# Kernel optimization log

Measured on AMD Instinct MI355X. Metric: run time of the kernel, lower is better.

## Reference

```python
import jax, jax.numpy as jnp
import numpy as np

H_DIM = 1024
HEAD_SIZE = 1024


def setup_inputs() -> dict:
    key = jax.random.key(0)
    ks = jax.random.split(key, 7)
    s = 1.0 / np.sqrt(H_DIM)
    x = jax.random.normal(ks[0], (4, 4096, H_DIM), dtype=jnp.float32)
    Wq = jax.random.uniform(ks[1], (H_DIM, HEAD_SIZE), jnp.float32, -s, s)
    bq = jax.random.uniform(ks[2], (HEAD_SIZE,), jnp.float32, -s, s)
    Wk = jax.random.uniform(ks[3], (H_DIM, HEAD_SIZE), jnp.float32, -s, s)
    bk = jax.random.uniform(ks[4], (HEAD_SIZE,), jnp.float32, -s, s)
    Wv = jax.random.uniform(ks[5], (H_DIM, HEAD_SIZE), jnp.float32, -s, s)
    bv = jax.random.uniform(ks[6], (HEAD_SIZE,), jnp.float32, -s, s)
    return {"x": x, "Wq": Wq, "bq": bq, "Wk": Wk, "bk": bk, "Wv": Wv, "bv": bv}


def reference(x, Wq, bq, Wk, bk, Wv, bv):
    B, S, _ = x.shape
    q = x @ Wq + bq  # [B,S,hs]
    k = x @ Wk + bk
    v = x @ Wv + bv
    scores = jnp.einsum('bqd,bkd->bqk', q, k)  # [B,S,S]
    causal = jnp.tril(jnp.ones((S, S), dtype=bool))
    scores = jnp.where(causal, scores, -jnp.inf)
    # original divides after masking; -inf stays -inf so math is identical
    w = jax.nn.softmax(scores / jnp.sqrt(jnp.float32(HEAD_SIZE)), axis=-1)
    # dropout p=0.0 -> identity
    return jnp.einsum('bqk,bkd->bqd', w, v)
```

## Files before the change

kernel.cpp:

```cpp
#include <hip/hip_runtime.h>
#include <stdint.h>

typedef _Float16 f16;
typedef _Float16 v8h __attribute__((ext_vector_type(8)));
typedef _Float16 v4h __attribute__((ext_vector_type(4)));
typedef float v4f __attribute__((ext_vector_type(4)));

#define LOG2E 1.44269504088896340736f
#define PT 16384

__device__ __forceinline__ void gll16(const void* g, void* l) {
  __builtin_amdgcn_global_load_lds((__attribute__((address_space(1))) void*)g,
                                   (__attribute__((address_space(3))) void*)l,
                                   16, 0, 0);
}

__device__ __forceinline__ int xcd_swz(int p, int chunk) {
  return (p & 7) * chunk + (p >> 3);
}

__global__ void k_cvt_x(const float* __restrict__ x, f16* __restrict__ xh, int n4) {
  int i = blockIdx.x * blockDim.x + threadIdx.x;
  if (i >= n4) return;
  float4 v = ((const float4*)x)[i];
  v4h o;
  o[0] = (f16)v.x; o[1] = (f16)v.y; o[2] = (f16)v.z; o[3] = (f16)v.w;
  ((v4h*)xh)[i] = o;
}

__global__ void k_cvt_wt(const float* __restrict__ Wq, const float* __restrict__ Wk,
                         const float* __restrict__ Wv, f16* __restrict__ Wt) {
  __shared__ f16 tile[64][65];
  int z = blockIdx.z;
  const float* W = (z == 0) ? Wq : (z == 1) ? Wk : Wv;
  int k0 = blockIdx.y * 64, n0 = blockIdx.x * 64;
  int t = threadIdx.x;
  int r = t >> 4, c4 = t & 15;
  for (int i = 0; i < 4; ++i) {
    int row = r + i * 16;
    float4 v = *(const float4*)&W[(size_t)(k0 + row) * 1024 + n0 + c4 * 4];
    tile[c4 * 4 + 0][row] = (f16)v.x;
    tile[c4 * 4 + 1][row] = (f16)v.y;
    tile[c4 * 4 + 2][row] = (f16)v.z;
    tile[c4 * 4 + 3][row] = (f16)v.w;
  }
  __syncthreads();
  f16* out = Wt + (size_t)z * 1048576;
  for (int i = 0; i < 4; ++i) {
    int n = r + i * 16;
    v4h o;
    o[0] = tile[n][c4 * 4 + 0];
    o[1] = tile[n][c4 * 4 + 1];
    o[2] = tile[n][c4 * 4 + 2];
    o[3] = tile[n][c4 * 4 + 3];
    *(v4h*)&out[(size_t)(n0 + n) * 1024 + k0 + c4 * 4] = o;
  }
}

__global__ __launch_bounds__(512) void k_qkv(
    const f16* __restrict__ xh,
    const f16* __restrict__ Wt,
    const float* __restrict__ bq, const float* __restrict__ bk, const float* __restrict__ bv,
    f16* __restrict__ q, f16* __restrict__ k, f16* __restrict__ vT) {
  __shared__ __align__(16) f16 As[2][16384];
  __shared__ __align__(16) f16 Bs[2][16384];
  int p = blockIdx.x + 64 * (blockIdx.y + 4 * blockIdx.z);
  int l = xcd_swz(p, 96);
  int mt = l / 12;
  int rem = l - mt * 12;
  int z = rem >> 2, nt = rem & 3;
  int m0 = mt * 256, n0 = nt * 256;
  const f16* gA = xh + (size_t)m0 * 1024;
  const f16* gB = Wt + (size_t)z * 1048576 + (size_t)n0 * 1024;
  const float* bias = (z == 0) ? bq : (z == 1) ? bk : bv;
  int tid = threadIdx.x;
  int lane = tid & 63, wave = tid >> 6;
  int quad = lane >> 4, l15 = lane & 15;
  int wm = (wave >> 2) * 128, wn = (wave & 3) * 64;

  int soff[4], slds[4];
#pragma unroll
  for (int h = 0; h < 4; ++h) {
    int s = h * 512 + tid;
    int row = s >> 3;
    int c = (s & 7) ^ (row & 7);
    soff[h] = row * 1024 + c * 8;
    slds[h] = (h * 512 + wave * 64) * 8;
  }
  v4f acc[8][4] = {};

#define QKV_STAGE(bb, kt_) do { int kk_ = (kt_) * 64;                      \
    _Pragma("unroll") for (int h = 0; h < 4; ++h)                          \
      gll16(gA + soff[h] + kk_, &As[bb][slds[h]]);                         \
    _Pragma("unroll") for (int h = 0; h < 4; ++h)                          \
      gll16(gB + soff[h] + kk_, &Bs[bb][slds[h]]);                         \
  } while (0)

#define QKV_COMPUTE(bb) do {                                               \
    _Pragma("unroll") for (int ks = 0; ks < 2; ++ks) {                     \
      int sl = ((ks * 4 + quad) ^ (l15 & 7)) * 8;                          \
      v8h a[8], bfr[4];                                                    \
      _Pragma("unroll") for (int i = 0; i < 8; ++i)                        \
        a[i] = *(const v8h*)&As[bb][(wm + i * 16 + l15) * 64 + sl];        \
      _Pragma("unroll") for (int j = 0; j < 4; ++j)                        \
        bfr[j] = *(const v8h*)&Bs[bb][(wn + j * 16 + l15) * 64 + sl];      \
      __builtin_amdgcn_s_setprio(1);                                       \
      _Pragma("unroll") for (int i = 0; i < 8; ++i)                        \
        _Pragma("unroll") for (int j = 0; j < 4; ++j)                      \
          acc[i][j] = __builtin_amdgcn_mfma_f32_16x16x32_f16(a[i], bfr[j], acc[i][j], 0, 0, 0); \
      __builtin_amdgcn_s_setprio(0);                                       \
      __builtin_amdgcn_s_barrier();                                        \
    }                                                                      \
  } while (0)

  QKV_STAGE(0, 0);
  QKV_STAGE(1, 1);
  int cur = 0;
#pragma unroll 1
  for (int kt = 0; kt < 15; ++kt) {
    asm volatile("s_waitcnt vmcnt(8)" ::: "memory");
    __builtin_amdgcn_s_barrier();
    QKV_COMPUTE(cur);
    if (kt + 2 < 16) QKV_STAGE(cur, kt + 2);
    cur ^= 1;
  }
  asm volatile("s_waitcnt vmcnt(0)" ::: "memory");
  __builtin_amdgcn_s_barrier();
  QKV_COMPUTE(cur);

  if (z < 2) {
    f16* outp = (z == 0) ? q : k;
    float scale = (z == 0) ? 0.03125f : 1.0f;
#pragma unroll
    for (int j = 0; j < 4; ++j) {
      int n = n0 + wn + j * 16 + l15;
      float bia = bias[n];
#pragma unroll
      for (int i = 0; i < 8; ++i) {
        int mb = m0 + wm + i * 16 + quad * 4;
#pragma unroll
        for (int r = 0; r < 4; ++r)
          outp[(size_t)(mb + r) * 1024 + n] = (f16)((acc[i][j][r] + bia) * scale);
      }
    }
  } else {
#pragma unroll
    for (int j = 0; j < 4; ++j) {
      int n = n0 + wn + j * 16 + l15;
      float bia = bias[n];
#pragma unroll
      for (int i = 0; i < 8; ++i) {
        int m = m0 + wm + i * 16 + quad * 4;
        int bb = m >> 12, s = m & 4095;
        v4h o;
#pragma unroll
        for (int r = 0; r < 4; ++r) o[r] = (f16)(acc[i][j][r] + bia);
        *(v4h*)&vT[((size_t)bb * 1024 + n) * 4096 + s] = o;
      }
    }
  }
#undef QKV_STAGE
#undef QKV_COMPUTE
}

__global__ void k_zero(float* __restrict__ p) {
  p[blockIdx.x * 256 + threadIdx.x] = 0.f;
}

__global__ __launch_bounds__(256) void k_sgemm(
    const f16* __restrict__ q, const f16* __restrict__ kmat,
    f16* __restrict__ P, float* __restrict__ rowsum, int b0) {
  __shared__ __align__(16) f16 As[128 * 32];
  __shared__ __align__(16) f16 Bs[128 * 32];
  int p = blockIdx.x + 528 * blockIdx.y;
  int l = xcd_swz(p, 132);
  int i = (l >= 528) ? l - 528 : l;
  int bb = (l >= 528) ? 1 : 0;
  int b = b0 * 2 + bb;
  int mt = (int)((sqrtf(8.f * i + 1.f) - 1.f) * 0.5f);
  while ((mt + 1) * (mt + 2) / 2 <= i) ++mt;
  while (mt * (mt + 1) / 2 > i) --mt;
  int nt = i - mt * (mt + 1) / 2;
  const f16* A = q + ((size_t)b * 4096 + (size_t)mt * 128) * 1024;
  const f16* B = kmat + ((size_t)b * 4096 + (size_t)nt * 128) * 1024;
  f16* Pt = P + (size_t)bb * 528 * PT + (size_t)i * PT;

  int tid = threadIdx.x;
  int lane = tid & 63, wave = tid >> 6;
  int quad = lane >> 4, l15 = lane & 15;
  int wm = (wave & 1) * 64, wn = (wave >> 1) * 64;
  v4f acc[4][4] = {};

  for (int kk = 0; kk < 1024; kk += 32) {
    __syncthreads();
    for (int h = 0; h < 2; ++h) {
      int s = h * 256 + tid;
      int row = s >> 2, pos = s & 3;
      int c = pos ^ (row & 3);
      gll16(&A[(size_t)row * 1024 + kk + c * 8], &As[(h * 256 + wave * 64) * 8]);
    }
    for (int h = 0; h < 2; ++h) {
      int s = h * 256 + tid;
      int row = s >> 2, pos = s & 3;
      int c = pos ^ (row & 3);
      gll16(&B[(size_t)row * 1024 + kk + c * 8], &Bs[(h * 256 + wave * 64) * 8]);
    }
    __syncthreads();
    v8h a[4], bf[4];
    for (int ii = 0; ii < 4; ++ii) {
      int rowa = wm + ii * 16 + l15;
      int pa = quad ^ (rowa & 3);
      a[ii] = *(const v8h*)&As[rowa * 32 + pa * 8];
      int rowb = wn + ii * 16 + l15;
      int pb = quad ^ (rowb & 3);
      bf[ii] = *(const v8h*)&Bs[rowb * 32 + pb * 8];
    }
    for (int ii = 0; ii < 4; ++ii)
      for (int j = 0; j < 4; ++j)
        acc[ii][j] = __builtin_amdgcn_mfma_f32_16x16x32_f16(a[ii], bf[j], acc[ii][j], 0, 0, 0);
  }

  bool diag = (nt == mt);
  float* rsb = rowsum + (size_t)b * 4096 + mt * 128;
  for (int ii = 0; ii < 4; ++ii) {
    int rl = wm + ii * 16 + quad * 4;
    for (int r = 0; r < 4; ++r) {
      int row_l = rl + r;
      float rs = 0.f;
      for (int j = 0; j < 4; ++j) {
        int col_l = wn + j * 16 + l15;
        float pv = __builtin_amdgcn_exp2f(acc[ii][j][r] * LOG2E);
        if (diag && col_l > row_l) pv = 0.f;
        Pt[(size_t)row_l * 128 + col_l] = (f16)pv;
        rs += pv;
      }
      rs += __shfl_xor(rs, 1, 64);
      rs += __shfl_xor(rs, 2, 64);
      rs += __shfl_xor(rs, 4, 64);
      rs += __shfl_xor(rs, 8, 64);
      if (l15 == 0) atomicAdd(&rsb[row_l], rs);
    }
  }
}

__global__ __launch_bounds__(256) void k_pv(
    const f16* __restrict__ P, const f16* __restrict__ vT,
    const float* __restrict__ rowsum, float* __restrict__ out, int b0) {
  __shared__ __align__(16) f16 As[128 * 64];
  __shared__ __align__(16) f16 Bs[64 * 64];
  int p = blockIdx.x + 16 * (blockIdx.y + 16 * blockIdx.z);
  int l = xcd_swz(p, 64);
  int dt = l & 15;
  int pr = (l >> 4) & 15;
  int bb = l >> 8;
  int b = b0 * 2 + bb;
  const f16* Pb = P + (size_t)bb * 528 * PT;
  const f16* Vb = vT + (size_t)b * 1024 * 4096;
  int tid = threadIdx.x;
  int lane = tid & 63, wave = tid >> 6;
  int quad = lane >> 4, l15 = lane & 15;
  int wm = (wave & 1) * 64, wn = (wave >> 1) * 32;

  for (int half = 0; half < 2; ++half) {
    int mt = half ? (31 - pr) : pr;
    size_t ptri = (size_t)mt * (mt + 1) / 2;
    v4f acc[4][2] = {};
    for (int kt = 0; kt <= mt; ++kt) {
      const f16* Ptile = Pb + (ptri + kt) * PT;
      int kabs = kt * 128;
      for (int kc = 0; kc < 128; kc += 64) {
        __syncthreads();
        for (int h = 0; h < 4; ++h) {
          int s = h * 256 + tid;
          int row = s >> 3, pos = s & 7;
          int c = pos ^ (row & 7);
          gll16(&Ptile[(size_t)row * 128 + kc + c * 8], &As[(h * 256 + wave * 64) * 8]);
        }
        for (int h = 0; h < 2; ++h) {
          int s = h * 256 + tid;
          int row = s >> 3, pos = s & 7;
          int c = pos ^ (row & 7);
          gll16(&Vb[(size_t)(dt * 64 + row) * 4096 + kabs + kc + c * 8],
                &Bs[(h * 256 + wave * 64) * 8]);
        }
        __syncthreads();
        for (int ks = 0; ks < 2; ++ks) {
          v8h a[4], bf[2];
          int lc = ks * 4 + quad;
          for (int ii = 0; ii < 4; ++ii) {
            int rowa = wm + ii * 16 + l15;
            a[ii] = *(const v8h*)&As[rowa * 64 + (lc ^ (rowa & 7)) * 8];
          }
          for (int j = 0; j < 2; ++j) {
            int rowb = wn + j * 16 + l15;
            bf[j] = *(const v8h*)&Bs[rowb * 64 + (lc ^ (rowb & 7)) * 8];
          }
          for (int ii = 0; ii < 4; ++ii)
            for (int j = 0; j < 2; ++j)
              acc[ii][j] = __builtin_amdgcn_mfma_f32_16x16x32_f16(a[ii], bf[j], acc[ii][j], 0, 0, 0);
        }
      }
    }
    const float* rsb = rowsum + (size_t)b * 4096 + mt * 128;
    float* ob = out + ((size_t)b * 4096 + (size_t)mt * 128) * 1024 + dt * 64;
    for (int ii = 0; ii < 4; ++ii) {
      int r0 = wm + ii * 16 + quad * 4;
      for (int r = 0; r < 4; ++r) {
        float inv = 1.0f / rsb[r0 + r];
        for (int j = 0; j < 2; ++j) {
          int c = wn + j * 16 + l15;
          ob[(size_t)(r0 + r) * 1024 + c] = acc[ii][j][r] * inv;
        }
      }
    }
  }
}

extern "C" void kernel_launch(void* const* d_in, const int* in_sizes, int n_in,
                              void* d_out, int out_size, void* d_ws, size_t ws_size,
                              hipStream_t stream) {
  const float* x  = (const float*)d_in[0];
  const float* Wq = (const float*)d_in[1];
  const float* bq = (const float*)d_in[2];
  const float* Wk = (const float*)d_in[3];
  const float* bk = (const float*)d_in[4];
  const float* Wv = (const float*)d_in[5];
  const float* bv = (const float*)d_in[6];
  float* out = (float*)d_out;
  char* ws = (char*)d_ws;
  f16* xh = (f16*)(ws);
  f16* Wt = (f16*)(ws + 33554432);
  f16* q  = (f16*)(ws + 39845888);
  f16* k  = (f16*)(ws + 73400320);
  f16* vT = (f16*)(ws + 106954752);
  f16* P  = (f16*)(ws);
  float* rowsum = (float*)(ws + 34603008);

  k_cvt_x<<<16384, 256, 0, stream>>>(x, xh, 4194304);
  k_cvt_wt<<<dim3(16, 16, 3), 256, 0, stream>>>(Wq, Wk, Wv, Wt);
  k_qkv<<<dim3(64, 4, 3), 512, 0, stream>>>(xh, Wt, bq, bk, bv, q, k, vT);
  k_zero<<<64, 256, 0, stream>>>(rowsum);
  for (int bp = 0; bp < 2; ++bp) {
    k_sgemm<<<dim3(528, 2), 256, 0, stream>>>(q, k, P, rowsum, bp);
    k_pv<<<dim3(16, 16, 2), 256, 0, stream>>>(P, vT, rowsum, out, bp);
  }
}
```

Baseline: 489.5 us.

## Interleave LDS reads, async prefetch and MFMA phases in QKV and PV kernels

The QKV GEMM main loop moves from a two-stage prefetch-ahead scheme to a one-ahead ping-pong. Each k-step is split into four quarter phases that use smaller fragment register sets, with the global->LDS loads for the next tile issued between phases. The PV kernel gains double-buffered LDS, precomputed swizzled offsets and the same interleaved prefetch schedule, replacing the sync-load-compute loop. This aims to hide load latency behind MFMA work and lower register pressure. The cost is more barriers, and QKV now waits on vmcnt(0) with a shallower prefetch depth.

```diff
diff --git a/kernel.cpp b/kernel.cpp
--- a/kernel.cpp
+++ b/kernel.cpp
@@ -87,46 +87,81 @@
     soff[h] = row * 1024 + c * 8;
     slds[h] = (h * 512 + wave * 64) * 8;
   }
+  int sl0 = (quad ^ (l15 & 7)) * 8;
+  int sl1 = ((4 + quad) ^ (l15 & 7)) * 8;
   v4f acc[8][4] = {};
 
-#define QKV_STAGE(bb, kt_) do { int kk_ = (kt_) * 64;                      \
-    _Pragma("unroll") for (int h = 0; h < 4; ++h)                          \
-      gll16(gA + soff[h] + kk_, &As[bb][slds[h]]);                         \
-    _Pragma("unroll") for (int h = 0; h < 4; ++h)                          \
-      gll16(gB + soff[h] + kk_, &Bs[bb][slds[h]]);                         \
-  } while (0)
-
-#define QKV_COMPUTE(bb) do {                                               \
-    _Pragma("unroll") for (int ks = 0; ks < 2; ++ks) {                     \
-      int sl = ((ks * 4 + quad) ^ (l15 & 7)) * 8;                          \
-      v8h a[8], bfr[4];                                                    \
-      _Pragma("unroll") for (int i = 0; i < 8; ++i)                        \
-        a[i] = *(const v8h*)&As[bb][(wm + i * 16 + l15) * 64 + sl];        \
-      _Pragma("unroll") for (int j = 0; j < 4; ++j)                        \
-        bfr[j] = *(const v8h*)&Bs[bb][(wn + j * 16 + l15) * 64 + sl];      \
-      __builtin_amdgcn_s_setprio(1);                                       \
-      _Pragma("unroll") for (int i = 0; i < 8; ++i)                        \
-        _Pragma("unroll") for (int j = 0; j < 4; ++j)                      \
-          acc[i][j] = __builtin_amdgcn_mfma_f32_16x16x32_f16(a[i], bfr[j], acc[i][j], 0, 0, 0); \
-      __builtin_amdgcn_s_setprio(0);                                       \
-      __builtin_amdgcn_s_barrier();                                        \
-    }                                                                      \
-  } while (0)
-
-  QKV_STAGE(0, 0);
-  QKV_STAGE(1, 1);
-  int cur = 0;
+#pragma unroll
+  for (int h = 0; h < 4; ++h) gll16(gA + soff[h], &As[0][slds[h]]);
+#pragma unroll
+  for (int h = 0; h < 4; ++h) gll16(gB + soff[h], &Bs[0][slds[h]]);
+
 #pragma unroll 1
-  for (int kt = 0; kt < 15; ++kt) {
-    asm volatile("s_waitcnt vmcnt(8)" ::: "memory");
-    __builtin_amdgcn_s_barrier();
-    QKV_COMPUTE(cur);
-    if (kt + 2 < 16) QKV_STAGE(cur, kt + 2);
-    cur ^= 1;
-  }
-  asm volatile("s_waitcnt vmcnt(0)" ::: "memory");
-  __builtin_amdgcn_s_barrier();
-  QKV_COMPUTE(cur);
+  for (int kt = 0; kt < 16; ++kt) {
+    f16* Ac = As[kt & 1];
+    f16* Bc = Bs[kt & 1];
+    f16* An = As[(kt & 1) ^ 1];
+    f16* Bn = Bs[(kt & 1) ^ 1];
+    int kn = (kt + 1) * 64;
+    asm volatile("s_waitcnt vmcnt(0)" ::: "memory");
+    __builtin_amdgcn_s_barrier();
+    v8h a[4], b_[4];
+#pragma unroll
+    for (int ii = 0; ii < 4; ++ii) a[ii] = *(const v8h*)&Ac[(wm + ii * 16 + l15) * 64 + sl0];
+#pragma unroll
+    for (int j = 0; j < 4; ++j) b_[j] = *(const v8h*)&Bc[(wn + j * 16 + l15) * 64 + sl0];
+    if (kt < 15) {
+#pragma unroll
+      for (int h = 0; h < 4; ++h) gll16(gA + soff[h] + kn, &An[slds[h]]);
+    }
+    __builtin_amdgcn_s_barrier();
+    __builtin_amdgcn_s_setprio(1);
+#pragma unroll
+    for (int ii = 0; ii < 4; ++ii)
+#pragma unroll
+      for (int j = 0; j < 4; ++j)
+        acc[ii][j] = __builtin_amdgcn_mfma_f32_16x16x32_f16(a[ii], b_[j], acc[ii][j], 0, 0, 0);
+    __builtin_amdgcn_s_setprio(0);
+    __builtin_amdgcn_s_barrier();
+#pragma unroll
+    for (int ii = 0; ii < 4; ++ii) a[ii] = *(const v8h*)&Ac[(wm + 64 + ii * 16 + l15) * 64 + sl0];
+    if (kt < 15) {
+#pragma unroll
+      for (int h = 0; h < 4; ++h) gll16(gB + soff[h] + kn, &Bn[slds[h]]);
+    }
+    __builtin_amdgcn_s_barrier();
+    __builtin_amdgcn_s_setprio(1);
+#pragma unroll
+    for (int ii = 0; ii < 4; ++ii)
+#pragma unroll
+      for (int j = 0; j < 4; ++j)
+        acc[4 + ii][j] = __builtin_amdgcn_mfma_f32_16x16x32_f16(a[ii], b_[j], acc[4 + ii][j], 0, 0, 0);
+    __builtin_amdgcn_s_setprio(0);
+    __builtin_amdgcn_s_barrier();
+#pragma unroll
+    for (int ii = 0; ii < 4; ++ii) a[ii] = *(const v8h*)&Ac[(wm + ii * 16 + l15) * 64 + sl1];
+#pragma unroll
+    for (int j = 0; j < 4; ++j) b_[j] = *(const v8h*)&Bc[(wn + j * 16 + l15) * 64 + sl1];
+    __builtin_amdgcn_s_barrier();
+    __builtin_amdgcn_s_setprio(1);
+#pragma unroll
+    for (int ii = 0; ii < 4; ++ii)
+#pragma unroll
+      for (int j = 0; j < 4; ++j)
+        acc[ii][j] = __builtin_amdgcn_mfma_f32_16x16x32_f16(a[ii], b_[j], acc[ii][j], 0, 0, 0);
+    __builtin_amdgcn_s_setprio(0);
+    __builtin_amdgcn_s_barrier();
+#pragma unroll
+    for (int ii = 0; ii < 4; ++ii) a[ii] = *(const v8h*)&Ac[(wm + 64 + ii * 16 + l15) * 64 + sl1];
+    __builtin_amdgcn_s_barrier();
+    __builtin_amdgcn_s_setprio(1);
+#pragma unroll
+    for (int ii = 0; ii < 4; ++ii)
+#pragma unroll
+      for (int j = 0; j < 4; ++j)
+        acc[4 + ii][j] = __builtin_amdgcn_mfma_f32_16x16x32_f16(a[ii], b_[j], acc[4 + ii][j], 0, 0, 0);
+    __builtin_amdgcn_s_setprio(0);
+  }
 
   if (z < 2) {
     f16* outp = (z == 0) ? q : k;
@@ -159,8 +194,6 @@
       }
     }
   }
-#undef QKV_STAGE
-#undef QKV_COMPUTE
 }
 
 __global__ void k_zero(float* __restrict__ p) {
@@ -246,8 +279,8 @@
 __global__ __launch_bounds__(256) void k_pv(
     const f16* __restrict__ P, const f16* __restrict__ vT,
     const float* __restrict__ rowsum, float* __restrict__ out, int b0) {
-  __shared__ __align__(16) f16 As[128 * 64];
-  __shared__ __align__(16) f16 Bs[64 * 64];
+  __shared__ __align__(16) f16 As[2][8192];
+  __shared__ __align__(16) f16 Bs[2][4096];
   int p = blockIdx.x + 16 * (blockIdx.y + 16 * blockIdx.z);
   int l = xcd_swz(p, 64);
   int dt = l & 15;
@@ -261,45 +294,81 @@
   int quad = lane >> 4, l15 = lane & 15;
   int wm = (wave & 1) * 64, wn = (wave >> 1) * 32;
 
+  int aoff[4], aslds[4];
+#pragma unroll
+  for (int h = 0; h < 4; ++h) {
+    int s = h * 256 + tid;
+    int row = s >> 3;
+    int c = (s & 7) ^ (row & 7);
+    aoff[h] = row * 128 + c * 8;
+    aslds[h] = (h * 256 + wave * 64) * 8;
+  }
+  int boff[2], bslds[2];
+#pragma unroll
+  for (int h = 0; h < 2; ++h) {
+    int s = h * 256 + tid;
+    int row = s >> 3;
+    int c = (s & 7) ^ (row & 7);
+    boff[h] = (size_t)0 + (dt * 64 + row) * 4096 + c * 8;
+    bslds[h] = (h * 256 + wave * 64) * 8;
+  }
+  int sl0 = (quad ^ (l15 & 7)) * 8;
+  int sl1 = ((4 + quad) ^ (l15 & 7)) * 8;
+
   for (int half = 0; half < 2; ++half) {
     int mt = half ? (31 - pr) : pr;
     size_t ptri = (size_t)mt * (mt + 1) / 2;
+    int S = 2 * (mt + 1);
     v4f acc[4][2] = {};
-    for (int kt = 0; kt <= mt; ++kt) {
-      const f16* Ptile = Pb + (ptri + kt) * PT;
-      int kabs = kt * 128;
-      for (int kc = 0; kc < 128; kc += 64) {
-        __syncthreads();
-        for (int h = 0; h < 4; ++h) {
-          int s = h * 256 + tid;
-          int row = s >> 3, pos = s & 7;
-          int c = pos ^ (row & 7);
-          gll16(&Ptile[(size_t)row * 128 + kc + c * 8], &As[(h * 256 + wave * 64) * 8]);
-        }
-        for (int h = 0; h < 2; ++h) {
-          int s = h * 256 + tid;
-          int row = s >> 3, pos = s & 7;
-          int c = pos ^ (row & 7);
-          gll16(&Vb[(size_t)(dt * 64 + row) * 4096 + kabs + kc + c * 8],
-                &Bs[(h * 256 + wave * 64) * 8]);
-        }
-        __syncthreads();
-        for (int ks = 0; ks < 2; ++ks) {
-          v8h a[4], bf[2];
-          int lc = ks * 4 + quad;
-          for (int ii = 0; ii < 4; ++ii) {
-            int rowa = wm + ii * 16 + l15;
-            a[ii] = *(const v8h*)&As[rowa * 64 + (lc ^ (rowa & 7)) * 8];
-          }
-          for (int j = 0; j < 2; ++j) {
-            int rowb = wn + j * 16 + l15;
-            bf[j] = *(const v8h*)&Bs[rowb * 64 + (lc ^ (rowb & 7)) * 8];
-          }
-          for (int ii = 0; ii < 4; ++ii)
-            for (int j = 0; j < 2; ++j)
-              acc[ii][j] = __builtin_amdgcn_mfma_f32_16x16x32_f16(a[ii], bf[j], acc[ii][j], 0, 0, 0);
-        }
-      }
+    __builtin_amdgcn_s_barrier();
+    {
+      const f16* Pt = Pb + ptri * PT;
+#pragma unroll
+      for (int h = 0; h < 4; ++h) gll16(Pt + aoff[h], &As[0][aslds[h]]);
+#pragma unroll
+      for (int h = 0; h < 2; ++h) gll16(Vb + boff[h], &Bs[0][bslds[h]]);
+    }
+#pragma unroll 1
+    for (int s = 0; s < S; ++s) {
+      int c = s & 1;
+      asm volatile("s_waitcnt vmcnt(0)" ::: "memory");
+      __builtin_amdgcn_s_barrier();
+      int kt1 = (s + 1) >> 1, kc1 = ((s + 1) & 1) * 64;
+      const f16* Ptn = Pb + (ptri + kt1) * PT;
+      v8h a[4], b_[2];
+#pragma unroll
+      for (int ii = 0; ii < 4; ++ii) a[ii] = *(const v8h*)&As[c][(wm + ii * 16 + l15) * 64 + sl0];
+#pragma unroll
+      for (int j = 0; j < 2; ++j) b_[j] = *(const v8h*)&Bs[c][(wn + j * 16 + l15) * 64 + sl0];
+      if (s + 1 < S) {
+#pragma unroll
+        for (int h = 0; h < 4; ++h) gll16(Ptn + aoff[h] + kc1, &As[c ^ 1][aslds[h]]);
+      }
+      __builtin_amdgcn_s_barrier();
+      __builtin_amdgcn_s_setprio(1);
+#pragma unroll
+      for (int ii = 0; ii < 4; ++ii)
+#pragma unroll
+        for (int j = 0; j < 2; ++j)
+          acc[ii][j] = __builtin_amdgcn_mfma_f32_16x16x32_f16(a[ii], b_[j], acc[ii][j], 0, 0, 0);
+      __builtin_amdgcn_s_setprio(0);
+      __builtin_amdgcn_s_barrier();
+#pragma unroll
+      for (int ii = 0; ii < 4; ++ii) a[ii] = *(const v8h*)&As[c][(wm + ii * 16 + l15) * 64 + sl1];
+#pragma unroll
+      for (int j = 0; j < 2; ++j) b_[j] = *(const v8h*)&Bs[c][(wn + j * 16 + l15) * 64 + sl1];
+      if (s + 1 < S) {
+#pragma unroll
+        for (int h = 0; h < 2; ++h) gll16(Vb + boff[h] + kt1 * 128 + kc1, &Bs[c ^ 1][bslds[h]]);
+      }
+      __builtin_amdgcn_s_barrier();
+      __builtin_amdgcn_s_setprio(1);
+#pragma unroll
+      for (int ii = 0; ii < 4; ++ii)
+#pragma unroll
+        for (int j = 0; j < 2; ++j)
+          acc[ii][j] = __builtin_amdgcn_mfma_f32_16x16x32_f16(a[ii], b_[j], acc[ii][j], 0, 0, 0);
+      __builtin_amdgcn_s_setprio(0);
     }
     const float* rsb = rowsum + (size_t)b * 4096 + mt * 128;
     float* ob = out + ((size_t)b * 4096 + (size_t)mt * 128) * 1024 + dt * 64;
@@ -308,8 +377,8 @@
       for (int r = 0; r < 4; ++r) {
         float inv = 1.0f / rsb[r0 + r];
         for (int j = 0; j < 2; ++j) {
-          int c = wn + j * 16 + l15;
-          ob[(size_t)(r0 + r) * 1024 + c] = acc[ii][j][r] * inv;
+          int cc = wn + j * 16 + l15;
+          ob[(size_t)(r0 + r) * 1024 + cc] = acc[ii][j][r] * inv;
         }
       }
     }
```

New measurement: 496.9 us. No clear change (+1.5%).

## Interleave split-stage LDS prefetch with MFMA in QKV and PV GEMMs

Applied to the files above, without the earlier changes.

Restructures the QKV projection main loop so the A and B halves of each next k-tile are issued at separate points between the two MFMA sub-steps, using double buffers that alternate each half-iteration. Also converts the PV kernel from a single-buffered, fully synchronized load-then-compute loop into a double-buffered pipeline with the same interleaved prefetch. The aim is to hide global-to-LDS latency behind matrix-core work and cut the number of full barriers per tile. The cost is double the LDS in the PV kernel, which may lower occupancy, plus delicate vmcnt counting and barrier placement.

```diff
diff --git a/kernel.cpp b/kernel.cpp
--- a/kernel.cpp
+++ b/kernel.cpp
@@ -88,45 +88,70 @@
     slds[h] = (h * 512 + wave * 64) * 8;
   }
   v4f acc[8][4] = {};
-
-#define QKV_STAGE(bb, kt_) do { int kk_ = (kt_) * 64;                      \
+  v8h a[8], bfr[4];
+
+#define QSTAGE(dst, g, kf) do {                                            \
     _Pragma("unroll") for (int h = 0; h < 4; ++h)                          \
-      gll16(gA + soff[h] + kk_, &As[bb][slds[h]]);                         \
-    _Pragma("unroll") for (int h = 0; h < 4; ++h)                          \
-      gll16(gB + soff[h] + kk_, &Bs[bb][slds[h]]);                         \
-  } while (0)
-
-#define QKV_COMPUTE(bb) do {                                               \
-    _Pragma("unroll") for (int ks = 0; ks < 2; ++ks) {                     \
-      int sl = ((ks * 4 + quad) ^ (l15 & 7)) * 8;                          \
-      v8h a[8], bfr[4];                                                    \
-      _Pragma("unroll") for (int i = 0; i < 8; ++i)                        \
-        a[i] = *(const v8h*)&As[bb][(wm + i * 16 + l15) * 64 + sl];        \
+      gll16((g) + soff[h] + (kf), &(dst)[slds[h]]);                        \
+  } while (0)
+
+#define QREAD(d, ks) do {                                                  \
+    int sl = (((ks) * 4 + quad) ^ (l15 & 7)) * 8;                          \
+    _Pragma("unroll") for (int i = 0; i < 8; ++i)                          \
+      a[i] = *(const v8h*)&As[d][(wm + i * 16 + l15) * 64 + sl];           \
+    _Pragma("unroll") for (int j = 0; j < 4; ++j)                          \
+      bfr[j] = *(const v8h*)&Bs[d][(wn + j * 16 + l15) * 64 + sl];         \
+  } while (0)
+
+#define QMFMA() do {                                                       \
+    __builtin_amdgcn_s_setprio(1);                                         \
+    _Pragma("unroll") for (int i = 0; i < 8; ++i)                          \
       _Pragma("unroll") for (int j = 0; j < 4; ++j)                        \
-        bfr[j] = *(const v8h*)&Bs[bb][(wn + j * 16 + l15) * 64 + sl];      \
-      __builtin_amdgcn_s_setprio(1);                                       \
-      _Pragma("unroll") for (int i = 0; i < 8; ++i)                        \
-        _Pragma("unroll") for (int j = 0; j < 4; ++j)                      \
-          acc[i][j] = __builtin_amdgcn_mfma_f32_16x16x32_f16(a[i], bfr[j], acc[i][j], 0, 0, 0); \
-      __builtin_amdgcn_s_setprio(0);                                       \
-      __builtin_amdgcn_s_barrier();                                        \
-    }                                                                      \
-  } while (0)
-
-  QKV_STAGE(0, 0);
-  QKV_STAGE(1, 1);
-  int cur = 0;
+        acc[i][j] = __builtin_amdgcn_mfma_f32_16x16x32_f16(a[i], bfr[j], acc[i][j], 0, 0, 0); \
+    __builtin_amdgcn_s_setprio(0);                                         \
+  } while (0)
+
+  QSTAGE(As[0], gA, 0);
+  QSTAGE(Bs[0], gB, 0);
+
 #pragma unroll 1
-  for (int kt = 0; kt < 15; ++kt) {
-    asm volatile("s_waitcnt vmcnt(8)" ::: "memory");
-    __builtin_amdgcn_s_barrier();
-    QKV_COMPUTE(cur);
-    if (kt + 2 < 16) QKV_STAGE(cur, kt + 2);
-    cur ^= 1;
-  }
-  asm volatile("s_waitcnt vmcnt(0)" ::: "memory");
-  __builtin_amdgcn_s_barrier();
-  QKV_COMPUTE(cur);
+  for (int it = 0; it < 7; ++it) {
+    int k1 = (2 * it + 1) * 64, k2 = (2 * it + 2) * 64;
+    QSTAGE(As[1], gA, k1);
+    asm volatile("s_waitcnt vmcnt(4)" ::: "memory");
+    __builtin_amdgcn_s_barrier();
+    QREAD(0, 0); QMFMA();
+    QREAD(0, 1);
+    QSTAGE(Bs[1], gB, k1);
+    QMFMA();
+    __builtin_amdgcn_s_barrier();
+    QSTAGE(As[0], gA, k2);
+    asm volatile("s_waitcnt vmcnt(4)" ::: "memory");
+    __builtin_amdgcn_s_barrier();
+    QREAD(1, 0); QMFMA();
+    QREAD(1, 1);
+    QSTAGE(Bs[0], gB, k2);
+    QMFMA();
+    __builtin_amdgcn_s_barrier();
+  }
+  {
+    int k1 = 15 * 64;
+    QSTAGE(As[1], gA, k1);
+    asm volatile("s_waitcnt vmcnt(4)" ::: "memory");
+    __builtin_amdgcn_s_barrier();
+    QREAD(0, 0); QMFMA();
+    QREAD(0, 1);
+    QSTAGE(Bs[1], gB, k1);
+    QMFMA();
+    __builtin_amdgcn_s_barrier();
+    asm volatile("s_waitcnt vmcnt(0)" ::: "memory");
+    __builtin_amdgcn_s_barrier();
+    QREAD(1, 0); QMFMA();
+    QREAD(1, 1); QMFMA();
+  }
+#undef QSTAGE
+#undef QREAD
+#undef QMFMA
 
   if (z < 2) {
     f16* outp = (z == 0) ? q : k;
@@ -159,8 +184,6 @@
       }
     }
   }
-#undef QKV_STAGE
-#undef QKV_COMPUTE
 }
 
 __global__ void k_zero(float* __restrict__ p) {
@@ -246,8 +269,8 @@
 __global__ __launch_bounds__(256) void k_pv(
     const f16* __restrict__ P, const f16* __restrict__ vT,
     const float* __restrict__ rowsum, float* __restrict__ out, int b0) {
-  __shared__ __align__(16) f16 As[128 * 64];
-  __shared__ __align__(16) f16 Bs[64 * 64];
+  __shared__ __align__(16) f16 As[2][8192];
+  __shared__ __align__(16) f16 Bs[2][4096];
   int p = blockIdx.x + 16 * (blockIdx.y + 16 * blockIdx.z);
   int l = xcd_swz(p, 64);
   int dt = l & 15;
@@ -261,45 +284,91 @@
   int quad = lane >> 4, l15 = lane & 15;
   int wm = (wave & 1) * 64, wn = (wave >> 1) * 32;
 
+  int aoff[4], aslds[4];
+#pragma unroll
+  for (int h = 0; h < 4; ++h) {
+    int s = h * 256 + tid;
+    int row = s >> 3;
+    int c = (s & 7) ^ (row & 7);
+    aoff[h] = row * 128 + c * 8;
+    aslds[h] = (h * 256 + wave * 64) * 8;
+  }
+  int boff[2], bslds[2];
+#pragma unroll
+  for (int h = 0; h < 2; ++h) {
+    int s = h * 256 + tid;
+    int row = s >> 3;
+    int c = (s & 7) ^ (row & 7);
+    boff[h] = (dt * 64 + row) * 4096 + c * 8;
+    bslds[h] = (h * 256 + wave * 64) * 8;
+  }
+  v8h a[4], b_[2];
+
+#define PSTAGE_A(d, Pt_, kc) do {                                          \
+    _Pragma("unroll") for (int h = 0; h < 4; ++h)                          \
+      gll16((Pt_) + aoff[h] + (kc), &As[d][aslds[h]]);                     \
+  } while (0)
+#define PSTAGE_B(d, koff) do {                                             \
+    _Pragma("unroll") for (int h = 0; h < 2; ++h)                          \
+      gll16(Vb + boff[h] + (koff), &Bs[d][bslds[h]]);                      \
+  } while (0)
+#define PREAD(d, ks) do {                                                  \
+    int sl = (((ks) * 4 + quad) ^ (l15 & 7)) * 8;                          \
+    _Pragma("unroll") for (int ii = 0; ii < 4; ++ii)                       \
+      a[ii] = *(const v8h*)&As[d][(wm + ii * 16 + l15) * 64 + sl];         \
+    _Pragma("unroll") for (int j = 0; j < 2; ++j)                          \
+      b_[j] = *(const v8h*)&Bs[d][(wn + j * 16 + l15) * 64 + sl];          \
+  } while (0)
+#define PMFMA(acc_) do {                                                   \
+    __builtin_amdgcn_s_setprio(1);                                         \
+    _Pragma("unroll") for (int ii = 0; ii < 4; ++ii)                       \
+      _Pragma("unroll") for (int j = 0; j < 2; ++j)                        \
+        acc_[ii][j] = __builtin_amdgcn_mfma_f32_16x16x32_f16(a[ii], b_[j], acc_[ii][j], 0, 0, 0); \
+    __builtin_amdgcn_s_setprio(0);                                         \
+  } while (0)
+
   for (int half = 0; half < 2; ++half) {
     int mt = half ? (31 - pr) : pr;
     size_t ptri = (size_t)mt * (mt + 1) / 2;
     v4f acc[4][2] = {};
-    for (int kt = 0; kt <= mt; ++kt) {
-      const f16* Ptile = Pb + (ptri + kt) * PT;
-      int kabs = kt * 128;
-      for (int kc = 0; kc < 128; kc += 64) {
-        __syncthreads();
-        for (int h = 0; h < 4; ++h) {
-          int s = h * 256 + tid;
-          int row = s >> 3, pos = s & 7;
-          int c = pos ^ (row & 7);
-          gll16(&Ptile[(size_t)row * 128 + kc + c * 8], &As[(h * 256 + wave * 64) * 8]);
-        }
-        for (int h = 0; h < 2; ++h) {
-          int s = h * 256 + tid;
-          int row = s >> 3, pos = s & 7;
-          int c = pos ^ (row & 7);
-          gll16(&Vb[(size_t)(dt * 64 + row) * 4096 + kabs + kc + c * 8],
-                &Bs[(h * 256 + wave * 64) * 8]);
-        }
-        __syncthreads();
-        for (int ks = 0; ks < 2; ++ks) {
-          v8h a[4], bf[2];
-          int lc = ks * 4 + quad;
-          for (int ii = 0; ii < 4; ++ii) {
-            int rowa = wm + ii * 16 + l15;
-            a[ii] = *(const v8h*)&As[rowa * 64 + (lc ^ (rowa & 7)) * 8];
-          }
-          for (int j = 0; j < 2; ++j) {
-            int rowb = wn + j * 16 + l15;
-            bf[j] = *(const v8h*)&Bs[rowb * 64 + (lc ^ (rowb & 7)) * 8];
-          }
-          for (int ii = 0; ii < 4; ++ii)
-            for (int j = 0; j < 2; ++j)
-              acc[ii][j] = __builtin_amdgcn_mfma_f32_16x16x32_f16(a[ii], bf[j], acc[ii][j], 0, 0, 0);
-        }
-      }
+    PSTAGE_A(0, Pb + ptri * PT, 0);
+    PSTAGE_B(0, 0);
+#pragma unroll 1
+    for (int i = 0; i < mt; ++i) {
+      const f16* Pti = Pb + (ptri + i) * PT;
+      const f16* Ptn = Pti + PT;
+      PSTAGE_A(1, Pti, 64);
+      asm volatile("s_waitcnt vmcnt(4)" ::: "memory");
+      __builtin_amdgcn_s_barrier();
+      PREAD(0, 0); PMFMA(acc);
+      PREAD(0, 1);
+      PSTAGE_B(1, i * 128 + 64);
+      PMFMA(acc);
+      __builtin_amdgcn_s_barrier();
+      PSTAGE_A(0, Ptn, 0);
+      asm volatile("s_waitcnt vmcnt(4)" ::: "memory");
+      __builtin_amdgcn_s_barrier();
+      PREAD(1, 0); PMFMA(acc);
+      PREAD(1, 1);
+      PSTAGE_B(0, (i + 1) * 128);
+      PMFMA(acc);
+      __builtin_amdgcn_s_barrier();
+    }
+    {
+      const f16* Pti = Pb + (ptri + mt) * PT;
+      PSTAGE_A(1, Pti, 64);
+      asm volatile("s_waitcnt vmcnt(4)" ::: "memory");
+      __builtin_amdgcn_s_barrier();
+      PREAD(0, 0); PMFMA(acc);
+      PREAD(0, 1);
+      PSTAGE_B(1, mt * 128 + 64);
+      PMFMA(acc);
+      __builtin_amdgcn_s_barrier();
+      asm volatile("s_waitcnt vmcnt(0)" ::: "memory");
+      __builtin_amdgcn_s_barrier();
+      PREAD(1, 0); PMFMA(acc);
+      PREAD(1, 1); PMFMA(acc);
+      __builtin_amdgcn_s_barrier();
     }
     const float* rsb = rowsum + (size_t)b * 4096 + mt * 128;
     float* ob = out + ((size_t)b * 4096 + (size_t)mt * 128) * 1024 + dt * 64;
@@ -308,12 +377,16 @@
       for (int r = 0; r < 4; ++r) {
         float inv = 1.0f / rsb[r0 + r];
         for (int j = 0; j < 2; ++j) {
-          int c = wn + j * 16 + l15;
-          ob[(size_t)(r0 + r) * 1024 + c] = acc[ii][j][r] * inv;
+          int cc = wn + j * 16 + l15;
+          ob[(size_t)(r0 + r) * 1024 + cc] = acc[ii][j][r] * inv;
         }
       }
     }
   }
+#undef PSTAGE_A
+#undef PSTAGE_B
+#undef PREAD
+#undef PMFMA
 }
 
 extern "C" void kernel_launch(void* const* d_in, const int* in_sizes, int n_in,
```

After: 472.4 us. 1.04x faster.
